# Optimization experiments

Hardware: AMD Instinct MI355X
Metric: run time of the kernel (lower is better)

Reference implementation:

```python
import jax, jax.numpy as jnp
import numpy as np

K = 3      # kernel_size
PAD = 1    # (dilation*(K-1)+1)//2 with dilation=1
EPS = 1e-3 # keras BatchNormalization default epsilon


def _unfold(x, k=K, pad=PAD):
    # reflect-pad local-window gather, torch.nn.functional.unfold ordering
    # x: [N,C,H,W] -> [N,C,k*k,H*W]
    N, C, H, W = x.shape
    xp = jnp.pad(x, ((0, 0), (0, 0), (pad, pad), (pad, pad)), mode='reflect')
    pats = jnp.stack([xp[:, :, i:i + H, j:j + W] for i in range(k) for j in range(k)], axis=2)
    return pats.reshape(N, C, k * k, H * W)


def _position(H, W):
    # [1,2,H,W]: channel 0 = x(-1..1 across W), channel 1 = y(-1..1 across H)
    loc_w = jnp.tile(jnp.linspace(-1.0, 1.0, W)[None, :], (H, 1))
    loc_h = jnp.tile(jnp.linspace(-1.0, 1.0, H)[:, None], (1, W))
    return jnp.stack([loc_w, loc_h], axis=0)[None].astype(jnp.float32)


def _bn(x, g, b, m, v):
    # keras BN, default axis=-1 (here the H*W axis), inference mode
    return (x - m) / jnp.sqrt(v + EPS) * g + b


def setup_inputs():
    key = jax.random.key(0)
    ks = jax.random.split(key, 16)
    N, C, H, W = 16, 256, 56, 56
    REL, OUT, SHARE = 16, 64, 8
    HW = H * W
    f = lambda k_, s: jax.random.normal(k_, s, dtype=jnp.float32)
    return {
        'x': f(ks[0], (N, C, H, W)),
        'conv1_w': f(ks[1], (REL, C)) * 0.05,
        'conv2_w': f(ks[2], (REL, C)) * 0.05,
        'conv3_w': f(ks[3], (OUT, C)) * 0.05,
        'convp_w': f(ks[4], (2, 2)),
        'convw1_w': f(ks[5], (REL, REL + 2)) * 0.2,
        'convw2_w': f(ks[6], (OUT // SHARE, REL)) * 0.2,
        'bn1_gamma': 1.0 + 0.1 * f(ks[7], (HW,)),
        'bn1_beta': 0.1 * f(ks[8], (HW,)),
        'bn1_mean': 0.1 * f(ks[9], (HW,)),
        'bn1_var': 1.0 + 0.5 * jax.random.uniform(ks[10], (HW,), dtype=jnp.float32),
        'bn2_gamma': 1.0 + 0.1 * f(ks[11], (HW,)),
        'bn2_beta': 0.1 * f(ks[12], (HW,)),
        'bn2_mean': 0.1 * f(ks[13], (HW,)),
        'bn2_var': 1.0 + 0.5 * jax.random.uniform(ks[14], (HW,), dtype=jnp.float32),
    }


def reference(x, conv1_w, conv2_w, conv3_w, convp_w, convw1_w, convw2_w,
              bn1_gamma, bn1_beta, bn1_mean, bn1_var,
              bn2_gamma, bn2_beta, bn2_mean, bn2_var):
    N, C, H, W = x.shape
    HW = H * W
    # 1x1 convs (channels_first) as channel contractions
    x1 = jnp.einsum('oc,nchw->nohw', conv1_w, x)
    x2 = jnp.einsum('oc,nchw->nohw', conv2_w, x)
    x3 = jnp.einsum('oc,nchw->nohw', conv3_w, x)
    p = jnp.einsum('oc,nchw->nohw', convp_w, _position(H, W))  # [1,2,H,W]
    # subtraction2(x1, x2): center feature minus windowed neighbors -> [N,rel,k^2,HW]
    sub2 = x1.reshape(N, -1, 1, HW) - _unfold(x2)
    # subtraction(p): relative positions -> [1,2,k^2,HW], tiled over batch
    subp = p.reshape(1, 2, 1, HW) - _unfold(p)
    rel = jnp.concatenate([sub2, jnp.tile(subp, (N, 1, 1, 1))], axis=1)  # [N,rel+2,k^2,HW]
    # conv_w: BN -> ReLU -> 1x1 conv -> BN -> ReLU -> 1x1 conv
    h = jax.nn.relu(_bn(rel, bn1_gamma, bn1_beta, bn1_mean, bn1_var))
    h = jnp.einsum('oc,ncjl->nojl', convw1_w, h)
    h = jax.nn.relu(_bn(h, bn2_gamma, bn2_beta, bn2_mean, bn2_var))
    h = jnp.einsum('oc,ncjl->nojl', convw2_w, h)  # [N,out//share,k^2,HW]
    w = jax.nn.softmax(h, axis=-2)                # softmax over the k^2 window axis
    # aggregation: weighted neighbor sum, weight channel shared by share_planes channels
    xu = _unfold(x3)                              # [N,out,k^2,HW]
    c_w = w.shape[1]
    xu = xu.reshape(N, -1, c_w, K * K, HW)        # channel c -> (c//c_w, c%c_w)
    out = jnp.einsum('ncjl,ngcjl->ngcl', w, xu)   # sum over window positions j
    return out.reshape(N, -1, H, W)
```

## Files before the change

### kernel.cpp

```cpp
#include <hip/hip_runtime.h>
#include <hip/hip_bf16.h>

typedef short bf16x8 __attribute__((ext_vector_type(8)));
typedef float floatx4 __attribute__((ext_vector_type(4)));
typedef unsigned short ushort4v __attribute__((ext_vector_type(4)));

#define HW 3136
#define NB 16
#define NPIX 50176

#define P_CP   0
#define P_W1   4
#define P_W2   292
#define P_FLAG 420
#define P_BN   424
#define PREP_FLOATS (424 + 4 * HW)

__device__ __forceinline__ unsigned short f2bf(float f) {
    unsigned int u = __float_as_uint(f);
    unsigned int r = (u + 0x7FFFu + ((u >> 16) & 1u)) >> 16;
    return (unsigned short)r;
}
__device__ __forceinline__ float bf2f(unsigned short u) {
    return __uint_as_float(((unsigned int)u) << 16);
}
__device__ __forceinline__ void unp8(uint4 u, float* o) {
    o[0] = bf2f((unsigned short)(u.x & 0xFFFFu)); o[1] = bf2f((unsigned short)(u.x >> 16));
    o[2] = bf2f((unsigned short)(u.y & 0xFFFFu)); o[3] = bf2f((unsigned short)(u.y >> 16));
    o[4] = bf2f((unsigned short)(u.z & 0xFFFFu)); o[5] = bf2f((unsigned short)(u.z >> 16));
    o[6] = bf2f((unsigned short)(u.w & 0xFFFFu)); o[7] = bf2f((unsigned short)(u.w >> 16));
}
__device__ __forceinline__ float ldp(const void* p, int i, int isb) {
    return isb ? bf2f(((const unsigned short*)p)[i]) : ((const float*)p)[i];
}

__device__ __forceinline__ int detect_bf16(const void* varp, int* sflag) {
    if (threadIdx.x == 0) {
        const unsigned short* p = (const unsigned short*)varp;
        int ok = 1;
        for (int i = 0; i < 64; ++i) {
            unsigned short v = p[2 * i];
            if (v < 0x3F80u || v > 0x3FC0u) { ok = 0; break; }
        }
        *sflag = ok;
    }
    __syncthreads();
    return *sflag;
}

__global__ __launch_bounds__(256) void proj_kernel(
    const void* __restrict__ x,
    const void* __restrict__ w1, const void* __restrict__ w2,
    const void* __restrict__ w3,
    const void* __restrict__ cpw, const void* __restrict__ cw1,
    const void* __restrict__ cw2,
    const void* __restrict__ b1g, const void* __restrict__ b1b,
    const void* __restrict__ b1m, const void* __restrict__ b1v,
    const void* __restrict__ b2g, const void* __restrict__ b2b,
    const void* __restrict__ b2m, const void* __restrict__ b2v,
    unsigned short* __restrict__ y,
    float* __restrict__ prep)
{
    __shared__ int sflag;
    const int isb = detect_bf16(b1v, &sflag);
    const int tid = threadIdx.x;

    if (blockIdx.x == 0) {
        for (int i = tid; i < 4;   i += 256) prep[P_CP + i] = ldp(cpw, i, isb);
        for (int i = tid; i < 288; i += 256) prep[P_W1 + i] = ldp(cw1, i, isb);
        for (int i = tid; i < 128; i += 256) prep[P_W2 + i] = ldp(cw2, i, isb);
        if (tid == 0) prep[P_FLAG] = isb ? 1.f : 0.f;
        for (int i = tid; i < HW; i += 256) {
            float a1 = ldp(b1g, i, isb) * rsqrtf(ldp(b1v, i, isb) + 1e-3f);
            float c1 = ldp(b1b, i, isb) - ldp(b1m, i, isb) * a1;
            float a2 = ldp(b2g, i, isb) * rsqrtf(ldp(b2v, i, isb) + 1e-3f);
            float c2 = ldp(b2b, i, isb) - ldp(b2m, i, isb) * a2;
            prep[P_BN + i]          = a1;
            prep[P_BN + HW + i]     = c1;
            prep[P_BN + 2 * HW + i] = a2;
            prep[P_BN + 3 * HW + i] = c2;
        }
    }

    const int b    = blockIdx.x;
    const int n    = b / 25, pb = b % 25;
    const int wave = tid >> 6, lane = tid & 63;
    const int rh   = wave >> 1;
    const int l0   = pb * 128 + (wave & 1) * 64;
    if (l0 >= HW) return;
    const int col = lane & 15, quad = lane >> 4;

    const void* wps[3];
    int ros[3];
    if (rh == 0) { wps[0] = w1; wps[1] = w2; wps[2] = w3; ros[0] = 0; ros[1] = 0; ros[2] = 0; }
    else         { wps[0] = w3; wps[1] = w3; wps[2] = w3; ros[0] = 16; ros[1] = 32; ros[2] = 48; }

    const size_t xoff = (size_t)n * 256 * HW + l0 + 4 * col;

    floatx4 acc[3][4];
    const floatx4 z4 = {0.f, 0.f, 0.f, 0.f};
    #pragma unroll
    for (int r = 0; r < 3; ++r)
        #pragma unroll
        for (int t = 0; t < 4; ++t) acc[r][t] = z4;

    #pragma unroll
    for (int q = 0; q < 8; ++q) {
        const int cbase = q * 32 + quad * 8;
        ushort4v ld[8];
        if (isb) {
            const unsigned short* xb = (const unsigned short*)x + xoff;
            #pragma unroll
            for (int j = 0; j < 8; ++j)
                ld[j] = *(const ushort4v*)(xb + (size_t)(cbase + j) * HW);
        } else {
            const float* xb = (const float*)x + xoff;
            #pragma unroll
            for (int j = 0; j < 8; ++j) {
                floatx4 f = *(const floatx4*)(xb + (size_t)(cbase + j) * HW);
                #pragma unroll
                for (int t = 0; t < 4; ++t) ld[j][t] = f2bf(f[t]);
            }
        }
        bf16x8 bt[4];
        #pragma unroll
        for (int t = 0; t < 4; ++t)
            #pragma unroll
            for (int j = 0; j < 8; ++j) bt[t][j] = (short)ld[j][t];

        #pragma unroll
        for (int r = 0; r < 3; ++r) {
            bf16x8 af;
            if (isb) {
                af = *(const bf16x8*)((const unsigned short*)wps[r] + (ros[r] + col) * 256 + cbase);
            } else {
                const float* fp = (const float*)wps[r] + (ros[r] + col) * 256 + cbase;
                #pragma unroll
                for (int j = 0; j < 8; ++j) af[j] = (short)f2bf(fp[j]);
            }
            #pragma unroll
            for (int t = 0; t < 4; ++t)
                acc[r][t] = __builtin_amdgcn_mfma_f32_16x16x32_bf16(af, bt[t], acc[r][t], 0, 0, 0);
        }
    }

    unsigned short* yb = y + ((size_t)n * HW + l0 + 4 * col) * 96 + rh * 48 + quad * 4;
    #pragma unroll
    for (int r = 0; r < 3; ++r)
        #pragma unroll
        for (int t = 0; t < 4; ++t) {
            ushort4v pk;
            #pragma unroll
            for (int g = 0; g < 4; ++g) pk[g] = f2bf(acc[r][t][g]);
            *(ushort4v*)(yb + (size_t)t * 96 + r * 16) = pk;
        }
}

template <typename WT>
__global__ __launch_bounds__(256, 4) void attn_w_kernel(
    const unsigned short* __restrict__ yT,
    const float* __restrict__ prep,
    WT* __restrict__ wbuf)
{
    const int tid = threadIdx.x;
    const int bid = blockIdx.x;
    const int pb = bid / 9;
    const int j  = bid - pb * 9;
    const int p  = pb * 256 + tid;
    const int n  = p / HW;
    const int l  = p - n * HW;
    const int h  = l / 56, w = l - h * 56;
    const int dy = j / 3 - 1, dx = (j % 3) - 1;
    int hh = h + dy; hh = (hh < 0) ? -hh : ((hh > 55) ? 110 - hh : hh);
    int ww = w + dx; ww = (ww < 0) ? -ww : ((ww > 55) ? 110 - ww : ww);
    const int nbr = hh * 56 + ww;

    const float a1 = prep[P_BN + l];
    const float c1 = prep[P_BN + HW + l];
    const float a2 = prep[P_BN + 2 * HW + l];
    const float c2 = prep[P_BN + 3 * HW + l];

    const unsigned short* y1p = yT + ((size_t)n * HW + l) * 96;
    const unsigned short* y2p = yT + ((size_t)n * HW + nbr) * 96 + 16;
    float y1f[16], y2f[16];
    unp8(*(const uint4*)y1p, y1f);       unp8(*(const uint4*)(y1p + 8), y1f + 8);
    unp8(*(const uint4*)y2p, y2f);       unp8(*(const uint4*)(y2p + 8), y2f + 8);

    float rel[18];
    #pragma unroll
    for (int c = 0; c < 16; ++c)
        rel[c] = fmaxf(fmaf(y1f[c] - y2f[c], a1, c1), 0.f);
    const float dlw = (float)(w - ww) * (2.0f / 55.0f);
    const float dlh = (float)(h - hh) * (2.0f / 55.0f);
    rel[16] = fmaxf(fmaf(prep[P_CP + 0] * dlw + prep[P_CP + 1] * dlh, a1, c1), 0.f);
    rel[17] = fmaxf(fmaf(prep[P_CP + 2] * dlw + prep[P_CP + 3] * dlh, a1, c1), 0.f);

    float h1[16];
    #pragma unroll
    for (int o = 0; o < 16; ++o) {
        float s = 0.f;
        #pragma unroll
        for (int c = 0; c < 18; ++c)
            s = fmaf(prep[P_W1 + o * 18 + c], rel[c], s);
        h1[o] = fmaxf(fmaf(s, a2, c2), 0.f);
    }
    float h2[8];
    #pragma unroll
    for (int o2 = 0; o2 < 8; ++o2) {
        float s = 0.f;
        #pragma unroll
        for (int o = 0; o < 16; ++o)
            s = fmaf(prep[P_W2 + o2 * 16 + o], h1[o], s);
        h2[o2] = s;
    }

    WT* wp = wbuf + ((size_t)p * 9 + j) * 8;
    if constexpr (sizeof(WT) == 4) {
        floatx4 v0 = {h2[0], h2[1], h2[2], h2[3]};
        floatx4 v1 = {h2[4], h2[5], h2[6], h2[7]};
        *(floatx4*)wp       = v0;
        *(floatx4*)(wp + 4) = v1;
    } else {
        uint4 pk;
        pk.x = (unsigned int)f2bf(h2[0]) | ((unsigned int)f2bf(h2[1]) << 16);
        pk.y = (unsigned int)f2bf(h2[2]) | ((unsigned int)f2bf(h2[3]) << 16);
        pk.z = (unsigned int)f2bf(h2[4]) | ((unsigned int)f2bf(h2[5]) << 16);
        pk.w = (unsigned int)f2bf(h2[6]) | ((unsigned int)f2bf(h2[7]) << 16);
        *(uint4*)wp = pk;
    }
}

template <typename WT>
__global__ __launch_bounds__(256, 3) void agg_kernel(
    const unsigned short* __restrict__ yT,
    const WT* __restrict__ wbuf,
    const float* __restrict__ prep,
    void* __restrict__ out)
{
    const int isb = prep[P_FLAG] != 0.f;
    const int b = blockIdx.x;
    const int n = b / 49;
    const int l = (b - n * 49) * 64 + (threadIdx.x & 63);
    const int cg = threadIdx.x >> 6;
    const int h = l / 56, w = l - h * 56;

    int nbr[9];
    #pragma unroll
    for (int dy = 0; dy < 3; ++dy)
        #pragma unroll
        for (int dx = 0; dx < 3; ++dx) {
            int hh = h + dy - 1; hh = (hh < 0) ? -hh : ((hh > 55) ? 110 - hh : hh);
            int ww = w + dx - 1; ww = (ww < 0) ? -ww : ((ww > 55) ? 110 - ww : ww);
            nbr[dy * 3 + dx] = hh * 56 + ww;
        }

    float wf[72];
    const WT* wp = wbuf + (size_t)(n * HW + l) * 72;
    if constexpr (sizeof(WT) == 4) {
        #pragma unroll
        for (int i = 0; i < 18; ++i)
            *(floatx4*)(wf + 4 * i) = *(const floatx4*)(wp + 4 * i);
    } else {
        #pragma unroll
        for (int i = 0; i < 9; ++i) {
            uint4 u = *(const uint4*)(wp + 8 * i);
            unp8(u, wf + 8 * i);
        }
    }

    float inv[8];
    #pragma unroll
    for (int c = 0; c < 8; ++c) {
        float m = wf[c];
        #pragma unroll
        for (int j = 1; j < 9; ++j) m = fmaxf(m, wf[j * 8 + c]);
        float s = 0.f;
        #pragma unroll
        for (int j = 0; j < 9; ++j) {
            float e = __expf(wf[j * 8 + c] - m);
            wf[j * 8 + c] = e;
            s += e;
        }
        inv[c] = 1.f / s;
    }

    const unsigned short* y3b = yT + (size_t)n * HW * 96 + 32 + cg * 16;
    float acc[16];
    #pragma unroll
    for (int cc = 0; cc < 16; ++cc) acc[cc] = 0.f;
    #pragma unroll
    for (int j = 0; j < 9; ++j) {
        const unsigned short* yp = y3b + (size_t)nbr[j] * 96;
        float yv[16];
        unp8(*(const uint4*)yp, yv);
        unp8(*(const uint4*)(yp + 8), yv + 8);
        #pragma unroll
        for (int cc = 0; cc < 16; ++cc)
            acc[cc] = fmaf(wf[j * 8 + (cc & 7)], yv[cc], acc[cc]);
    }

    const size_t obase = ((size_t)n * 64 + cg * 16) * HW + l;
    #pragma unroll
    for (int cc = 0; cc < 16; ++cc) {
        float v = acc[cc] * inv[cc & 7];
        if (isb) ((unsigned short*)out)[obase + (size_t)cc * HW] = f2bf(v);
        else     ((float*)out)[obase + (size_t)cc * HW]          = v;
    }
}

extern "C" void kernel_launch(void* const* d_in, const int* in_sizes, int n_in,
                              void* d_out, int out_size, void* d_ws, size_t ws_size,
                              hipStream_t stream)
{
    const size_t yB    = (size_t)NB * HW * 96 * 2;
    const size_t wB32  = (size_t)NPIX * 72 * 4;
    const size_t wB16  = (size_t)NPIX * 72 * 2;
    const size_t prepB = (size_t)PREP_FLOATS * 4;

    const bool w32 = ws_size >= yB + wB32 + prepB;
    unsigned short* y = (unsigned short*)d_ws;
    char* wsp = (char*)d_ws + yB;
    float* prep = (float*)((char*)d_ws + yB + (w32 ? wB32 : wB16));

    proj_kernel<<<dim3(400), dim3(256), 0, stream>>>(
        d_in[0], d_in[1], d_in[2], d_in[3],
        d_in[4], d_in[5], d_in[6],
        d_in[7], d_in[8], d_in[9], d_in[10],
        d_in[11], d_in[12], d_in[13], d_in[14],
        y, prep);

    if (w32) {
        float* wb = (float*)wsp;
        attn_w_kernel<float><<<dim3(1764), dim3(256), 0, stream>>>(y, prep, wb);
        agg_kernel<float><<<dim3(784), dim3(256), 0, stream>>>(y, wb, prep, d_out);
    } else {
        unsigned short* wb = (unsigned short*)wsp;
        attn_w_kernel<unsigned short><<<dim3(1764), dim3(256), 0, stream>>>(y, prep, wb);
        agg_kernel<unsigned short><<<dim3(784), dim3(256), 0, stream>>>(y, wb, prep, d_out);
    }
}
```

Before: 166.8 us.

## Fuse attention-weight and aggregation kernels via shared memory; pipeline projection loads

Merges the attention-weight computation, softmax and aggregation into a single kernel that keeps the 9x8 per-pixel weights in LDS. This removes the global weight buffer write and re-read. The projection kernel is reorganised into 384-thread blocks of 64 pixels, each wave covering two output row tiles, with double-buffered register staging of the x and weight loads. The fused kernel uses 576-thread blocks with about 25KB of LDS, which may limit occupancy, and the projection now does narrower 2-pixel loads per lane.

New measurement: 165.6 us. No clear change (-0.7%).

```diff
diff --git a/kernel.cpp b/kernel.cpp
--- a/kernel.cpp
+++ b/kernel.cpp
@@ -1,5 +1,4 @@
 #include <hip/hip_runtime.h>
-#include <hip/hip_bf16.h>
 
 typedef short bf16x8 __attribute__((ext_vector_type(8)));
 typedef float floatx4 __attribute__((ext_vector_type(4)));
@@ -7,7 +6,6 @@
 
 #define HW 3136
 #define NB 16
-#define NPIX 50176
 
 #define P_CP   0
 #define P_W1   4
@@ -15,6 +13,8 @@
 #define P_FLAG 420
 #define P_BN   424
 #define PREP_FLOATS (424 + 4 * HW)
+
+#define WS 100
 
 __device__ __forceinline__ unsigned short f2bf(float f) {
     unsigned int u = __float_as_uint(f);
@@ -48,7 +48,39 @@
     return *sflag;
 }
 
-__global__ __launch_bounds__(256) void proj_kernel(
+struct Stage { unsigned int b[8]; bf16x8 a[2]; };
+
+__device__ __forceinline__ void load_stage(
+    int isb, const void* x, size_t xbase, int cb,
+    const void* const (&wsA)[2], const int (&roA)[2], int col, Stage& st)
+{
+    if (isb) {
+        const unsigned short* xb = (const unsigned short*)x;
+        #pragma unroll
+        for (int j = 0; j < 8; ++j)
+            st.b[j] = *(const unsigned int*)(xb + xbase + (size_t)(cb + j) * HW);
+        #pragma unroll
+        for (int rt = 0; rt < 2; ++rt)
+            st.a[rt] = *(const bf16x8*)((const unsigned short*)wsA[rt] + (roA[rt] + col) * 256 + cb);
+    } else {
+        const float* xb = (const float*)x;
+        #pragma unroll
+        for (int j = 0; j < 8; ++j) {
+            float2 f = *(const float2*)(xb + xbase + (size_t)(cb + j) * HW);
+            st.b[j] = (unsigned int)f2bf(f.x) | ((unsigned int)f2bf(f.y) << 16);
+        }
+        #pragma unroll
+        for (int rt = 0; rt < 2; ++rt) {
+            const float* fp = (const float*)wsA[rt] + (roA[rt] + col) * 256 + cb;
+            bf16x8 af;
+            #pragma unroll
+            for (int j = 0; j < 8; ++j) af[j] = (short)f2bf(fp[j]);
+            st.a[rt] = af;
+        }
+    }
+}
+
+__global__ __launch_bounds__(384) void proj_kernel(
     const void* __restrict__ x,
     const void* __restrict__ w1, const void* __restrict__ w2,
     const void* __restrict__ w3,
@@ -66,11 +98,11 @@
     const int tid = threadIdx.x;
 
     if (blockIdx.x == 0) {
-        for (int i = tid; i < 4;   i += 256) prep[P_CP + i] = ldp(cpw, i, isb);
-        for (int i = tid; i < 288; i += 256) prep[P_W1 + i] = ldp(cw1, i, isb);
-        for (int i = tid; i < 128; i += 256) prep[P_W2 + i] = ldp(cw2, i, isb);
+        for (int i = tid; i < 4;   i += 384) prep[P_CP + i] = ldp(cpw, i, isb);
+        for (int i = tid; i < 288; i += 384) prep[P_W1 + i] = ldp(cw1, i, isb);
+        for (int i = tid; i < 128; i += 384) prep[P_W2 + i] = ldp(cw2, i, isb);
         if (tid == 0) prep[P_FLAG] = isb ? 1.f : 0.f;
-        for (int i = tid; i < HW; i += 256) {
+        for (int i = tid; i < HW; i += 384) {
             float a1 = ldp(b1g, i, isb) * rsqrtf(ldp(b1v, i, isb) + 1e-3f);
             float c1 = ldp(b1b, i, isb) - ldp(b1m, i, isb) * a1;
             float a2 = ldp(b2g, i, isb) * rsqrtf(ldp(b2v, i, isb) + 1e-3f);
@@ -82,229 +114,187 @@
         }
     }
 
-    const int b    = blockIdx.x;
-    const int n    = b / 25, pb = b % 25;
+    const int blk  = blockIdx.x;
+    const int n    = blk / 49;
     const int wave = tid >> 6, lane = tid & 63;
-    const int rh   = wave >> 1;
-    const int l0   = pb * 128 + (wave & 1) * 64;
-    if (l0 >= HW) return;
-    const int col = lane & 15, quad = lane >> 4;
-
-    const void* wps[3];
-    int ros[3];
-    if (rh == 0) { wps[0] = w1; wps[1] = w2; wps[2] = w3; ros[0] = 0; ros[1] = 0; ros[2] = 0; }
-    else         { wps[0] = w3; wps[1] = w3; wps[2] = w3; ros[0] = 16; ros[1] = 32; ros[2] = 48; }
-
-    const size_t xoff = (size_t)n * 256 * HW + l0 + 4 * col;
-
-    floatx4 acc[3][4];
+    const int s    = wave & 1;
+    const int rg   = wave >> 1;
+    const int col  = lane & 15, quad = lane >> 4;
+    const int lb   = (blk - n * 49) * 64 + s * 32;
+    const int px   = lb + 2 * col;
+
+    const void* wsA[2]; int roA[2];
+    if (rg == 0)      { wsA[0] = w1; roA[0] = 0;  wsA[1] = w2; roA[1] = 0;  }
+    else if (rg == 1) { wsA[0] = w3; roA[0] = 0;  wsA[1] = w3; roA[1] = 16; }
+    else              { wsA[0] = w3; roA[0] = 32; wsA[1] = w3; roA[1] = 48; }
+
+    const size_t xbase = (size_t)n * 256 * HW + px;
+
+    floatx4 acc[2][2];
     const floatx4 z4 = {0.f, 0.f, 0.f, 0.f};
     #pragma unroll
-    for (int r = 0; r < 3; ++r)
-        #pragma unroll
-        for (int t = 0; t < 4; ++t) acc[r][t] = z4;
-
+    for (int rt = 0; rt < 2; ++rt)
+        #pragma unroll
+        for (int t = 0; t < 2; ++t) acc[rt][t] = z4;
+
+    Stage st[2];
+    load_stage(isb, x, xbase, quad * 8, wsA, roA, col, st[0]);
     #pragma unroll
     for (int q = 0; q < 8; ++q) {
-        const int cbase = q * 32 + quad * 8;
-        ushort4v ld[8];
-        if (isb) {
-            const unsigned short* xb = (const unsigned short*)x + xoff;
-            #pragma unroll
-            for (int j = 0; j < 8; ++j)
-                ld[j] = *(const ushort4v*)(xb + (size_t)(cbase + j) * HW);
-        } else {
-            const float* xb = (const float*)x + xoff;
-            #pragma unroll
-            for (int j = 0; j < 8; ++j) {
-                floatx4 f = *(const floatx4*)(xb + (size_t)(cbase + j) * HW);
-                #pragma unroll
-                for (int t = 0; t < 4; ++t) ld[j][t] = f2bf(f[t]);
-            }
-        }
-        bf16x8 bt[4];
-        #pragma unroll
-        for (int t = 0; t < 4; ++t)
-            #pragma unroll
-            for (int j = 0; j < 8; ++j) bt[t][j] = (short)ld[j][t];
-
-        #pragma unroll
-        for (int r = 0; r < 3; ++r) {
-            bf16x8 af;
-            if (isb) {
-                af = *(const bf16x8*)((const unsigned short*)wps[r] + (ros[r] + col) * 256 + cbase);
-            } else {
-                const float* fp = (const float*)wps[r] + (ros[r] + col) * 256 + cbase;
-                #pragma unroll
-                for (int j = 0; j < 8; ++j) af[j] = (short)f2bf(fp[j]);
-            }
-            #pragma unroll
-            for (int t = 0; t < 4; ++t)
-                acc[r][t] = __builtin_amdgcn_mfma_f32_16x16x32_bf16(af, bt[t], acc[r][t], 0, 0, 0);
-        }
-    }
-
-    unsigned short* yb = y + ((size_t)n * HW + l0 + 4 * col) * 96 + rh * 48 + quad * 4;
+        if (q < 7)
+            load_stage(isb, x, xbase, (q + 1) * 32 + quad * 8, wsA, roA, col, st[(q + 1) & 1]);
+        Stage& c = st[q & 1];
+        bf16x8 bt0, bt1;
+        #pragma unroll
+        for (int j = 0; j < 8; ++j) {
+            bt0[j] = (short)(c.b[j] & 0xFFFFu);
+            bt1[j] = (short)(c.b[j] >> 16);
+        }
+        #pragma unroll
+        for (int rt = 0; rt < 2; ++rt) {
+            acc[rt][0] = __builtin_amdgcn_mfma_f32_16x16x32_bf16(c.a[rt], bt0, acc[rt][0], 0, 0, 0);
+            acc[rt][1] = __builtin_amdgcn_mfma_f32_16x16x32_bf16(c.a[rt], bt1, acc[rt][1], 0, 0, 0);
+        }
+    }
+
+    unsigned short* yb = y + ((size_t)n * HW + px) * 96 + rg * 32 + quad * 4;
     #pragma unroll
-    for (int r = 0; r < 3; ++r)
-        #pragma unroll
-        for (int t = 0; t < 4; ++t) {
+    for (int rt = 0; rt < 2; ++rt)
+        #pragma unroll
+        for (int t = 0; t < 2; ++t) {
             ushort4v pk;
             #pragma unroll
-            for (int g = 0; g < 4; ++g) pk[g] = f2bf(acc[r][t][g]);
-            *(ushort4v*)(yb + (size_t)t * 96 + r * 16) = pk;
-        }
-}
-
-template <typename WT>
-__global__ __launch_bounds__(256, 4) void attn_w_kernel(
+            for (int g = 0; g < 4; ++g) pk[g] = f2bf(acc[rt][t][g]);
+            *(ushort4v*)(yb + (size_t)t * 96 + rt * 16) = pk;
+        }
+}
+
+__global__ __launch_bounds__(576) void attn_kernel(
     const unsigned short* __restrict__ yT,
-    const float* __restrict__ prep,
-    WT* __restrict__ wbuf)
-{
-    const int tid = threadIdx.x;
-    const int bid = blockIdx.x;
-    const int pb = bid / 9;
-    const int j  = bid - pb * 9;
-    const int p  = pb * 256 + tid;
-    const int n  = p / HW;
-    const int l  = p - n * HW;
-    const int h  = l / 56, w = l - h * 56;
-    const int dy = j / 3 - 1, dx = (j % 3) - 1;
-    int hh = h + dy; hh = (hh < 0) ? -hh : ((hh > 55) ? 110 - hh : hh);
-    int ww = w + dx; ww = (ww < 0) ? -ww : ((ww > 55) ? 110 - ww : ww);
-    const int nbr = hh * 56 + ww;
-
-    const float a1 = prep[P_BN + l];
-    const float c1 = prep[P_BN + HW + l];
-    const float a2 = prep[P_BN + 2 * HW + l];
-    const float c2 = prep[P_BN + 3 * HW + l];
-
-    const unsigned short* y1p = yT + ((size_t)n * HW + l) * 96;
-    const unsigned short* y2p = yT + ((size_t)n * HW + nbr) * 96 + 16;
-    float y1f[16], y2f[16];
-    unp8(*(const uint4*)y1p, y1f);       unp8(*(const uint4*)(y1p + 8), y1f + 8);
-    unp8(*(const uint4*)y2p, y2f);       unp8(*(const uint4*)(y2p + 8), y2f + 8);
-
-    float rel[18];
-    #pragma unroll
-    for (int c = 0; c < 16; ++c)
-        rel[c] = fmaxf(fmaf(y1f[c] - y2f[c], a1, c1), 0.f);
-    const float dlw = (float)(w - ww) * (2.0f / 55.0f);
-    const float dlh = (float)(h - hh) * (2.0f / 55.0f);
-    rel[16] = fmaxf(fmaf(prep[P_CP + 0] * dlw + prep[P_CP + 1] * dlh, a1, c1), 0.f);
-    rel[17] = fmaxf(fmaf(prep[P_CP + 2] * dlw + prep[P_CP + 3] * dlh, a1, c1), 0.f);
-
-    float h1[16];
-    #pragma unroll
-    for (int o = 0; o < 16; ++o) {
-        float s = 0.f;
-        #pragma unroll
-        for (int c = 0; c < 18; ++c)
-            s = fmaf(prep[P_W1 + o * 18 + c], rel[c], s);
-        h1[o] = fmaxf(fmaf(s, a2, c2), 0.f);
-    }
-    float h2[8];
-    #pragma unroll
-    for (int o2 = 0; o2 < 8; ++o2) {
-        float s = 0.f;
-        #pragma unroll
-        for (int o = 0; o < 16; ++o)
-            s = fmaf(prep[P_W2 + o2 * 16 + o], h1[o], s);
-        h2[o2] = s;
-    }
-
-    WT* wp = wbuf + ((size_t)p * 9 + j) * 8;
-    if constexpr (sizeof(WT) == 4) {
-        floatx4 v0 = {h2[0], h2[1], h2[2], h2[3]};
-        floatx4 v1 = {h2[4], h2[5], h2[6], h2[7]};
-        *(floatx4*)wp       = v0;
-        *(floatx4*)(wp + 4) = v1;
-    } else {
-        uint4 pk;
-        pk.x = (unsigned int)f2bf(h2[0]) | ((unsigned int)f2bf(h2[1]) << 16);
-        pk.y = (unsigned int)f2bf(h2[2]) | ((unsigned int)f2bf(h2[3]) << 16);
-        pk.z = (unsigned int)f2bf(h2[4]) | ((unsigned int)f2bf(h2[5]) << 16);
-        pk.w = (unsigned int)f2bf(h2[6]) | ((unsigned int)f2bf(h2[7]) << 16);
-        *(uint4*)wp = pk;
-    }
-}
-
-template <typename WT>
-__global__ __launch_bounds__(256, 3) void agg_kernel(
-    const unsigned short* __restrict__ yT,
-    const WT* __restrict__ wbuf,
     const float* __restrict__ prep,
     void* __restrict__ out)
 {
+    __shared__ float wsm[64 * WS];
+    const int tid = threadIdx.x;
+    const int blk = blockIdx.x;
+    const int n   = blk / 49;
+    const int l0  = (blk - n * 49) * 64;
     const int isb = prep[P_FLAG] != 0.f;
-    const int b = blockIdx.x;
-    const int n = b / 49;
-    const int l = (b - n * 49) * 64 + (threadIdx.x & 63);
-    const int cg = threadIdx.x >> 6;
-    const int h = l / 56, w = l - h * 56;
-
-    int nbr[9];
-    #pragma unroll
-    for (int dy = 0; dy < 3; ++dy)
-        #pragma unroll
-        for (int dx = 0; dx < 3; ++dx) {
-            int hh = h + dy - 1; hh = (hh < 0) ? -hh : ((hh > 55) ? 110 - hh : hh);
-            int ww = w + dx - 1; ww = (ww < 0) ? -ww : ((ww > 55) ? 110 - ww : ww);
-            nbr[dy * 3 + dx] = hh * 56 + ww;
-        }
-
-    float wf[72];
-    const WT* wp = wbuf + (size_t)(n * HW + l) * 72;
-    if constexpr (sizeof(WT) == 4) {
-        #pragma unroll
-        for (int i = 0; i < 18; ++i)
-            *(floatx4*)(wf + 4 * i) = *(const floatx4*)(wp + 4 * i);
-    } else {
-        #pragma unroll
-        for (int i = 0; i < 9; ++i) {
-            uint4 u = *(const uint4*)(wp + 8 * i);
-            unp8(u, wf + 8 * i);
-        }
-    }
-
-    float inv[8];
-    #pragma unroll
-    for (int c = 0; c < 8; ++c) {
-        float m = wf[c];
-        #pragma unroll
-        for (int j = 1; j < 9; ++j) m = fmaxf(m, wf[j * 8 + c]);
+
+    {
+        const int j = tid >> 6;
+        const int p = tid & 63;
+        const int l = l0 + p;
+        const int h = l / 56, w = l - h * 56;
+        const int dy = j / 3 - 1, dx = j - (j / 3) * 3 - 1;
+        int hh = h + dy; hh = (hh < 0) ? -hh : ((hh > 55) ? 110 - hh : hh);
+        int ww = w + dx; ww = (ww < 0) ? -ww : ((ww > 55) ? 110 - ww : ww);
+        const int nbr = hh * 56 + ww;
+
+        const float a1 = prep[P_BN + l];
+        const float c1 = prep[P_BN + HW + l];
+        const float a2 = prep[P_BN + 2 * HW + l];
+        const float c2 = prep[P_BN + 3 * HW + l];
+
+        const unsigned short* y1p = yT + ((size_t)n * HW + l) * 96;
+        const unsigned short* y2p = yT + ((size_t)n * HW + nbr) * 96 + 16;
+        float y1f[16], y2f[16];
+        unp8(*(const uint4*)y1p, y1f);       unp8(*(const uint4*)(y1p + 8), y1f + 8);
+        unp8(*(const uint4*)y2p, y2f);       unp8(*(const uint4*)(y2p + 8), y2f + 8);
+
+        float rel[18];
+        #pragma unroll
+        for (int c = 0; c < 16; ++c)
+            rel[c] = fmaxf(fmaf(y1f[c] - y2f[c], a1, c1), 0.f);
+        const float dlw = (float)(w - ww) * (2.0f / 55.0f);
+        const float dlh = (float)(h - hh) * (2.0f / 55.0f);
+        rel[16] = fmaxf(fmaf(prep[P_CP + 0] * dlw + prep[P_CP + 1] * dlh, a1, c1), 0.f);
+        rel[17] = fmaxf(fmaf(prep[P_CP + 2] * dlw + prep[P_CP + 3] * dlh, a1, c1), 0.f);
+
+        float h1[16];
+        #pragma unroll
+        for (int o = 0; o < 16; ++o) {
+            float s = 0.f;
+            #pragma unroll
+            for (int c = 0; c < 18; ++c)
+                s = fmaf(prep[P_W1 + o * 18 + c], rel[c], s);
+            h1[o] = fmaxf(fmaf(s, a2, c2), 0.f);
+        }
+        float h2[8];
+        #pragma unroll
+        for (int o2 = 0; o2 < 8; ++o2) {
+            float s = 0.f;
+            #pragma unroll
+            for (int o = 0; o < 16; ++o)
+                s = fmaf(prep[P_W2 + o2 * 16 + o], h1[o], s);
+            h2[o2] = s;
+        }
+        float* wp = &wsm[p * WS + j * 8];
+        *(floatx4*)wp       = *(floatx4*)&h2[0];
+        *(floatx4*)(wp + 4) = *(floatx4*)&h2[4];
+    }
+    __syncthreads();
+
+    if (tid < 512) {
+        const int c = tid & 7, p = tid >> 3;
+        float v[9];
+        #pragma unroll
+        for (int j = 0; j < 9; ++j) v[j] = wsm[p * WS + j * 8 + c];
+        float m = v[0];
+        #pragma unroll
+        for (int j = 1; j < 9; ++j) m = fmaxf(m, v[j]);
         float s = 0.f;
         #pragma unroll
+        for (int j = 0; j < 9; ++j) { v[j] = __expf(v[j] - m); s += v[j]; }
+        const float inv = 1.f / s;
+        #pragma unroll
+        for (int j = 0; j < 9; ++j) wsm[p * WS + j * 8 + c] = v[j] * inv;
+    }
+    __syncthreads();
+
+    if (tid < 512) {
+        const int p  = tid & 63;
+        const int k8 = tid >> 6;
+        const int l = l0 + p;
+        const int h = l / 56, w = l - h * 56;
+        int nbr[9];
+        #pragma unroll
+        for (int dy = 0; dy < 3; ++dy)
+            #pragma unroll
+            for (int dx = 0; dx < 3; ++dx) {
+                int hh = h + dy - 1; hh = (hh < 0) ? -hh : ((hh > 55) ? 110 - hh : hh);
+                int ww = w + dx - 1; ww = (ww < 0) ? -ww : ((ww > 55) ? 110 - ww : ww);
+                nbr[dy * 3 + dx] = hh * 56 + ww;
+            }
+        const unsigned short* y3b = yT + (size_t)n * HW * 96 + 32 + k8 * 8;
+        float acc8[8];
+        #pragma unroll
+        for (int k = 0; k < 8; ++k) acc8[k] = 0.f;
+        #pragma unroll
         for (int j = 0; j < 9; ++j) {
-            float e = __expf(wf[j * 8 + c] - m);
-            wf[j * 8 + c] = e;
-            s += e;
-        }
-        inv[c] = 1.f / s;
-    }
-
-    const unsigned short* y3b = yT + (size_t)n * HW * 96 + 32 + cg * 16;
-    float acc[16];
-    #pragma unroll
-    for (int cc = 0; cc < 16; ++cc) acc[cc] = 0.f;
-    #pragma unroll
-    for (int j = 0; j < 9; ++j) {
-        const unsigned short* yp = y3b + (size_t)nbr[j] * 96;
-        float yv[16];
-        unp8(*(const uint4*)yp, yv);
-        unp8(*(const uint4*)(yp + 8), yv + 8);
-        #pragma unroll
-        for (int cc = 0; cc < 16; ++cc)
-            acc[cc] = fmaf(wf[j * 8 + (cc & 7)], yv[cc], acc[cc]);
-    }
-
-    const size_t obase = ((size_t)n * 64 + cg * 16) * HW + l;
-    #pragma unroll
-    for (int cc = 0; cc < 16; ++cc) {
-        float v = acc[cc] * inv[cc & 7];
-        if (isb) ((unsigned short*)out)[obase + (size_t)cc * HW] = f2bf(v);
-        else     ((float*)out)[obase + (size_t)cc * HW]          = v;
+            uint4 u = *(const uint4*)(y3b + (size_t)nbr[j] * 96);
+            float yv[8];
+            unp8(u, yv);
+            const float* wp = &wsm[p * WS + j * 8];
+            float2 w01 = *(const float2*)wp;
+            float2 w23 = *(const float2*)(wp + 2);
+            float2 w45 = *(const float2*)(wp + 4);
+            float2 w67 = *(const float2*)(wp + 6);
+            acc8[0] = fmaf(w01.x, yv[0], acc8[0]);
+            acc8[1] = fmaf(w01.y, yv[1], acc8[1]);
+            acc8[2] = fmaf(w23.x, yv[2], acc8[2]);
+            acc8[3] = fmaf(w23.y, yv[3], acc8[3]);
+            acc8[4] = fmaf(w45.x, yv[4], acc8[4]);
+            acc8[5] = fmaf(w45.y, yv[5], acc8[5]);
+            acc8[6] = fmaf(w67.x, yv[6], acc8[6]);
+            acc8[7] = fmaf(w67.y, yv[7], acc8[7]);
+        }
+        const size_t obase = ((size_t)n * 64 + k8 * 8) * HW + l;
+        #pragma unroll
+        for (int k = 0; k < 8; ++k) {
+            if (isb) ((unsigned short*)out)[obase + (size_t)k * HW] = f2bf(acc8[k]);
+            else     ((float*)out)[obase + (size_t)k * HW]          = acc8[k];
+        }
     }
 }
 
@@ -312,30 +302,16 @@
                               void* d_out, int out_size, void* d_ws, size_t ws_size,
                               hipStream_t stream)
 {
-    const size_t yB    = (size_t)NB * HW * 96 * 2;
-    const size_t wB32  = (size_t)NPIX * 72 * 4;
-    const size_t wB16  = (size_t)NPIX * 72 * 2;
-    const size_t prepB = (size_t)PREP_FLOATS * 4;
-
-    const bool w32 = ws_size >= yB + wB32 + prepB;
+    const size_t yB = (size_t)NB * HW * 96 * 2;
     unsigned short* y = (unsigned short*)d_ws;
-    char* wsp = (char*)d_ws + yB;
-    float* prep = (float*)((char*)d_ws + yB + (w32 ? wB32 : wB16));
-
-    proj_kernel<<<dim3(400), dim3(256), 0, stream>>>(
+    float* prep = (float*)((char*)d_ws + yB);
+
+    proj_kernel<<<dim3(784), dim3(384), 0, stream>>>(
         d_in[0], d_in[1], d_in[2], d_in[3],
         d_in[4], d_in[5], d_in[6],
         d_in[7], d_in[8], d_in[9], d_in[10],
         d_in[11], d_in[12], d_in[13], d_in[14],
         y, prep);
 
-    if (w32) {
-        float* wb = (float*)wsp;
-        attn_w_kernel<float><<<dim3(1764), dim3(256), 0, stream>>>(y, prep, wb);
-        agg_kernel<float><<<dim3(784), dim3(256), 0, stream>>>(y, wb, prep, d_out);
-    } else {
-        unsigned short* wb = (unsigned short*)wsp;
-        attn_w_kernel<unsigned short><<<dim3(1764), dim3(256), 0, stream>>>(y, prep, wb);
-        agg_kernel<unsigned short><<<dim3(784), dim3(256), 0, stream>>>(y, wb, prep, d_out);
-    }
-}
+    attn_kernel<<<dim3(784), dim3(576), 0, stream>>>(y, prep, d_out);
+}
```
